# Optimization experiments

Measured on AMD Instinct MI355X. Metric: run time of the kernel, lower is better.

## Reference

```python
import jax, jax.numpy as jnp
import numpy as np

B, D, H = 8192, 512, 512


def _linear_init(key, out_dim, in_dim, bias=True):
    # torch nn.Linear default: U(-1/sqrt(in_dim), 1/sqrt(in_dim)) for W and b
    k1, k2 = jax.random.split(key)
    bound = 1.0 / np.sqrt(in_dim)
    W = jax.random.uniform(k1, (out_dim, in_dim), jnp.float32, -bound, bound)
    if not bias:
        return W
    b = jax.random.uniform(k2, (out_dim,), jnp.float32, -bound, bound)
    return W, b


def setup_inputs() -> dict:
    key = jax.random.key(0)
    ks = jax.random.split(key, 16)
    x = jax.random.normal(ks[0], (B, D), jnp.float32)
    delta_t = jax.random.uniform(ks[1], (B, 1), jnp.float32)
    hidden = jax.random.normal(ks[2], (B, H), jnp.float32)
    cell_s = jax.random.normal(ks[3], (B, H), jnp.float32)
    Wii, bii = _linear_init(ks[4], H, D)
    Whi, bhi = _linear_init(ks[5], H, H)
    Wig, big = _linear_init(ks[6], H, D)
    Whg, bhg = _linear_init(ks[7], H, H)
    Wio, bio = _linear_init(ks[8], H, D)
    Who, bho = _linear_init(ks[9], H, H)
    Wto, bto = _linear_init(ks[10], H, 1)
    Wco, bco = _linear_init(ks[11], H, H)
    Wit1, bit1 = _linear_init(ks[12], H, D)
    Wtt1 = _linear_init(ks[13], H, 1, bias=False)
    Wit2, bit2 = _linear_init(ks[14], H, D)
    Wtt2 = _linear_init(ks[15], H, 1, bias=False)
    return dict(x=x, delta_t=delta_t, hidden=hidden, cell_s=cell_s,
                Wii=Wii, bii=bii, Whi=Whi, bhi=bhi, Wig=Wig, big=big,
                Whg=Whg, bhg=bhg, Wio=Wio, bio=bio, Who=Who, bho=bho,
                Wto=Wto, bto=bto, Wco=Wco, bco=bco, Wit1=Wit1, bit1=bit1,
                Wtt1=Wtt1, Wit2=Wit2, bit2=bit2, Wtt2=Wtt2)


def _lin(a, W, b=None):
    y = a @ W.T
    return y if b is None else y + b


def reference(x, delta_t, hidden, cell_s,
              Wii, bii, Whi, bhi, Wig, big, Whg, bhg,
              Wio, bio, Who, bho, Wto, bto, Wco, bco,
              Wit1, bit1, Wtt1, Wit2, bit2, Wtt2):
    sig, tanh = jax.nn.sigmoid, jnp.tanh
    tm1 = sig(_lin(x, Wit1, bit1) + sig(_lin(delta_t, Wtt1)))
    tm2 = sig(_lin(x, Wit2, bit2) + sig(_lin(delta_t, Wtt2)))
    im = sig(_lin(x, Wii, bii) + _lin(hidden, Whi, bhi))
    cur_in = tanh(_lin(x, Wig, big) + _lin(hidden, Whg, bhg))
    it1 = im * tm1
    cm_t = (1.0 - it1) * cell_s + it1 * cur_in
    cm = (1.0 - im) * cell_s + im * tm2 * cur_in
    om = sig(_lin(x, Wio, bio) + _lin(delta_t, Wto, bto)
             + _lin(hidden, Who, bho) + _lin(cm_t, Wco, bco))
    hm = om * tanh(cm_t)
    return (hm, cm)
```

## Files before the change

kernel.cpp:

```cpp
#include <hip/hip_runtime.h>
#include <hip/hip_bf16.h>
#include <stdint.h>

#define B_SZ 8192
#define D_SZ 512
#define H_SZ 512
#define KC 1024
#define NPRE 2560

typedef __attribute__((ext_vector_type(8))) __bf16 bf16x8;
typedef __attribute__((ext_vector_type(4))) float f32x4;

__device__ __forceinline__ unsigned short f2bf(float f) {
  unsigned u = __builtin_bit_cast(unsigned, f);
  u += 0x7FFFu + ((u >> 16) & 1u);
  return (unsigned short)(u >> 16);
}
__device__ __forceinline__ float bf2f(unsigned short h) {
  unsigned u = ((unsigned)h) << 16;
  return __builtin_bit_cast(float, u);
}
__device__ __forceinline__ float sigf(float x) { return 1.0f / (1.0f + __expf(-x)); }

__device__ __forceinline__ void async_ld16(const unsigned short* g, unsigned short* l) {
  __builtin_amdgcn_global_load_lds(
      (const __attribute__((address_space(1))) unsigned int*)g,
      (__attribute__((address_space(3))) unsigned int*)l, 16, 0, 0);
}

struct WSrcs { const float* wx[5]; const float* wh[3]; const float* wco; };

__global__ void pack_all(const float* __restrict__ x, const float* __restrict__ h, WSrcs ws,
                         unsigned short* __restrict__ Ab, unsigned short* __restrict__ Wall,
                         unsigned short* __restrict__ Wcob) {
  int i = (blockIdx.x * 256 + threadIdx.x) * 4;
  const int XH = B_SZ * KC;
  const float* s;
  unsigned short* d;
  if (i < XH) {
    int b = i >> 10, c = i & 1023;
    s = (c < 512) ? (x + (size_t)b * 512 + c) : (h + (size_t)b * 512 + (c - 512));
    d = Ab + i;
  } else if (i < XH + NPRE * KC) {
    int j = i - XH;
    int row = j >> 10, c = j & 1023;
    int gate = row >> 9, r = row & 511;
    d = Wall + j;
    if (c < 512) {
      s = ws.wx[gate] + (size_t)r * 512 + c;
    } else if (gate >= 2) {
      s = ws.wh[gate - 2] + (size_t)r * 512 + (c - 512);
    } else {
      return;
    }
  } else {
    int j = i - XH - NPRE * KC;
    s = ws.wco + j;
    d = Wcob + j;
  }
  float4 v = *(const float4*)s;
  ushort4 o; o.x = f2bf(v.x); o.y = f2bf(v.y); o.z = f2bf(v.z); o.w = f2bf(v.w);
  *(ushort4*)d = o;
}

__global__ __launch_bounds__(256, 2) void gemm_t12(
    const unsigned short* __restrict__ A, const unsigned short* __restrict__ W,
    unsigned short* __restrict__ T12,
    const float* __restrict__ bit1, const float* __restrict__ Wtt1,
    const float* __restrict__ bit2, const float* __restrict__ Wtt2,
    const float* __restrict__ delta_t) {
  __shared__ bf16x8 sA[128 * 8];
  __shared__ bf16x8 sW[128 * 8];
  const int tid  = threadIdx.x;
  const int wave = tid >> 6, lane = tid & 63;
  const int ln15 = lane & 15, kq = lane >> 4;
  const int wr = wave >> 1, wc = wave & 1;
  const long bm = (long)blockIdx.y * 128;
  const long bn = (long)blockIdx.x * 128;

  f32x4 acc[4][4];
#pragma unroll
  for (int i = 0; i < 4; ++i)
#pragma unroll
    for (int j = 0; j < 4; ++j) acc[i][j] = (f32x4){0.f, 0.f, 0.f, 0.f};

  const int swb = ln15 & 7;
  for (int kt = 0; kt < 8; ++kt) {
    const int k0 = kt << 6;
    __syncthreads();
#pragma unroll
    for (int it = 0; it < 4; ++it) {
      int f   = it * 256 + tid;
      int row = f >> 3;
      int col = ((f & 7) ^ (row & 7)) << 3;
      int ldsc = it * 256 + wave * 64;
      async_ld16(A + (size_t)(bm + row) * KC + k0 + col, (unsigned short*)sA + (size_t)ldsc * 8);
      async_ld16(W + (size_t)(bn + row) * KC + k0 + col, (unsigned short*)sW + (size_t)ldsc * 8);
    }
    __syncthreads();
#pragma unroll
    for (int ko = 0; ko < 2; ++ko) {
      const int q = (ko * 4 + kq) ^ swb;
      bf16x8 af[4], wf[4];
#pragma unroll
      for (int t = 0; t < 4; ++t)
        af[t] = sA[(wr * 64 + t * 16 + ln15) * 8 + q];
#pragma unroll
      for (int t = 0; t < 4; ++t)
        wf[t] = sW[(wc * 64 + t * 16 + ln15) * 8 + q];
#pragma unroll
      for (int i = 0; i < 4; ++i)
#pragma unroll
        for (int j = 0; j < 4; ++j)
          acc[i][j] = __builtin_amdgcn_mfma_f32_16x16x32_bf16(af[i], wf[j], acc[i][j], 0, 0, 0);
    }
  }
  const float* bitp = (bn < 512) ? bit1 : bit2;
  const float* wttp = (bn < 512) ? Wtt1 : Wtt2;
#pragma unroll
  for (int i = 0; i < 4; ++i) {
    const long r0 = bm + wr * 64 + i * 16 + kq * 4;
#pragma unroll
    for (int j = 0; j < 4; ++j) {
      const long c = bn + wc * 64 + j * 16 + ln15;
      const int hc = (int)c & 511;
      const float bv = bitp[hc], wv = wttp[hc];
#pragma unroll
      for (int r = 0; r < 4; ++r) {
        const long row = r0 + r;
        float v = sigf(acc[i][j][r] + bv + sigf(delta_t[row] * wv));
        T12[(size_t)row * 1024 + c] = f2bf(v);
      }
    }
  }
}

__global__ __launch_bounds__(384, 2) void igo_gate(
    const unsigned short* __restrict__ A, const unsigned short* __restrict__ Wigo,
    const unsigned short* __restrict__ T12,
    const float* __restrict__ delta_t, const float* __restrict__ cell_s,
    const float* __restrict__ bii, const float* __restrict__ bhi,
    const float* __restrict__ big, const float* __restrict__ bhg,
    const float* __restrict__ bio, const float* __restrict__ bho,
    const float* __restrict__ Wto, const float* __restrict__ bto,
    const float* __restrict__ bco,
    float* __restrict__ out_cm, unsigned short* __restrict__ cmt_b,
    unsigned short* __restrict__ ao_b) {
  __shared__ __align__(16) unsigned short sBuf[24576];
  const int tid  = threadIdx.x;
  const int wave = tid >> 6, lane = tid & 63;
  const int ln15 = lane & 15, kq = lane >> 4;
  const int mh   = wave / 3, slot = wave % 3;
  const long bm  = (long)blockIdx.y * 128;
  const int  bn64 = blockIdx.x * 64;

  f32x4 acc[4][4];
#pragma unroll
  for (int i = 0; i < 4; ++i)
#pragma unroll
    for (int j = 0; j < 4; ++j) acc[i][j] = (f32x4){0.f, 0.f, 0.f, 0.f};

  const int swb = ln15 & 7;
  bf16x8* chunks = (bf16x8*)sBuf;

  for (int kt = 0; kt < 16; ++kt) {
    const int k0 = kt << 6;
    __syncthreads();
#pragma unroll
    for (int it = 0; it < 7; ++it) {
      int idx = it * 384 + tid;
      if (idx < 2560) {
        int t   = idx >> 9;
        int f   = idx & 511;
        int row = f >> 3;
        int col = ((f & 7) ^ (row & 7)) << 3;
        const unsigned short* src;
        if (t < 2) src = A    + (size_t)(bm + t * 64 + row) * KC + k0 + col;
        else       src = Wigo + (size_t)((t - 2) * 512 + bn64 + row) * KC + k0 + col;
        async_ld16(src, sBuf + (size_t)idx * 8);
      }
    }
    __syncthreads();
#pragma unroll
    for (int ko = 0; ko < 2; ++ko) {
      const int q = (ko * 4 + kq) ^ swb;
      bf16x8 af[4], wf[4];
#pragma unroll
      for (int t = 0; t < 4; ++t)
        af[t] = chunks[mh * 512 + (t * 16 + ln15) * 8 + q];
#pragma unroll
      for (int t = 0; t < 4; ++t)
        wf[t] = chunks[(2 + slot) * 512 + (t * 16 + ln15) * 8 + q];
#pragma unroll
      for (int i = 0; i < 4; ++i)
#pragma unroll
        for (int j = 0; j < 4; ++j)
          acc[i][j] = __builtin_amdgcn_mfma_f32_16x16x32_bf16(af[i], wf[j], acc[i][j], 0, 0, 0);
    }
  }

  __syncthreads();
#pragma unroll
  for (int i = 0; i < 4; ++i)
#pragma unroll
    for (int j = 0; j < 4; ++j)
#pragma unroll
      for (int r = 0; r < 4; ++r) {
        int row = i * 16 + kq * 4 + r;
        int col = j * 16 + ln15;
        sBuf[(size_t)(mh * 3 + slot) * 4096 + row * 64 + col] = f2bf(acc[i][j][r]);
      }
  __syncthreads();

  for (int e4 = tid * 4; e4 < 8192; e4 += 384 * 4) {
    int emh = e4 >> 12;
    int rc  = e4 & 4095;
    int row = rc >> 6;
    int col = rc & 63;
    long b  = bm + emh * 64 + row;
    int  h  = bn64 + col;
    ushort4 uai = *(const ushort4*)(sBuf + (size_t)(emh * 3 + 0) * 4096 + row * 64 + col);
    ushort4 uag = *(const ushort4*)(sBuf + (size_t)(emh * 3 + 1) * 4096 + row * 64 + col);
    ushort4 uao = *(const ushort4*)(sBuf + (size_t)(emh * 3 + 2) * 4096 + row * 64 + col);
    ushort4 ut1 = *(const ushort4*)(T12 + (size_t)b * 1024 + h);
    ushort4 ut2 = *(const ushort4*)(T12 + (size_t)b * 1024 + 512 + h);
    float4 cs   = *(const float4*)(cell_s + (size_t)b * 512 + h);
    float4 vbii = *(const float4*)(bii + h), vbhi = *(const float4*)(bhi + h);
    float4 vbig = *(const float4*)(big + h), vbhg = *(const float4*)(bhg + h);
    float4 vbio = *(const float4*)(bio + h), vbho = *(const float4*)(bho + h);
    float4 vWto = *(const float4*)(Wto + h), vbto = *(const float4*)(bto + h);
    float4 vbco = *(const float4*)(bco + h);
    float dtb   = delta_t[b];

    float4 ocm; ushort4 ocmt, oao;
#pragma unroll
    for (int l = 0; l < 4; ++l) {
      float ai = bf2f(((const unsigned short*)&uai)[l]) + ((const float*)&vbii)[l] + ((const float*)&vbhi)[l];
      float ag = bf2f(((const unsigned short*)&uag)[l]) + ((const float*)&vbig)[l] + ((const float*)&vbhg)[l];
      float ao = bf2f(((const unsigned short*)&uao)[l]) + ((const float*)&vbio)[l] + ((const float*)&vbho)[l]
               + dtb * ((const float*)&vWto)[l] + ((const float*)&vbto)[l] + ((const float*)&vbco)[l];
      float t1 = bf2f(((const unsigned short*)&ut1)[l]);
      float t2 = bf2f(((const unsigned short*)&ut2)[l]);
      float im = sigf(ai);
      float g  = tanhf(ag);
      float csl = ((const float*)&cs)[l];
      float it1 = im * t1;
      float cmt = (1.f - it1) * csl + it1 * g;
      float cm  = (1.f - im) * csl + im * t2 * g;
      ((float*)&ocm)[l] = cm;
      ((unsigned short*)&ocmt)[l] = f2bf(cmt);
      ((unsigned short*)&oao)[l]  = f2bf(ao);
    }
    *(float4*)(out_cm + (size_t)b * 512 + h) = ocm;
    *(ushort4*)(cmt_b + (size_t)b * 512 + h) = ocmt;
    *(ushort4*)(ao_b  + (size_t)b * 512 + h) = oao;
  }
}

__global__ __launch_bounds__(256, 2) void gemm_out(
    const unsigned short* __restrict__ A , const unsigned short* __restrict__ W ,
    const unsigned short* __restrict__ AO, float* __restrict__ out_hm) {
  __shared__ bf16x8 sA[128 * 8];
  __shared__ bf16x8 sW[128 * 8];
  const int tid  = threadIdx.x;
  const int wave = tid >> 6, lane = tid & 63;
  const int ln15 = lane & 15, kq = lane >> 4;
  const int wr = wave >> 1, wc = wave & 1;
  const long bm = (long)blockIdx.y * 128;
  const long bn = (long)blockIdx.x * 128;
  const int swb = ln15 & 7;

  f32x4 acc[4][4];
#pragma unroll
  for (int i = 0; i < 4; ++i)
#pragma unroll
    for (int j = 0; j < 4; ++j) acc[i][j] = (f32x4){0.f, 0.f, 0.f, 0.f};

  for (int kt = 0; kt < 8; ++kt) {
    const int k0 = kt << 6;
    __syncthreads();
#pragma unroll
    for (int it = 0; it < 4; ++it) {
      int f   = it * 256 + tid;
      int row = f >> 3;
      int col = ((f & 7) ^ (row & 7)) << 3;
      int ldsc = it * 256 + wave * 64;
      async_ld16(A + (size_t)(bm + row) * H_SZ + k0 + col, (unsigned short*)sA + (size_t)ldsc * 8);
      async_ld16(W + (size_t)(bn + row) * H_SZ + k0 + col, (unsigned short*)sW + (size_t)ldsc * 8);
    }
    __syncthreads();
#pragma unroll
    for (int ko = 0; ko < 2; ++ko) {
      const int q = (ko * 4 + kq) ^ swb;
      bf16x8 af[4], wf[4];
#pragma unroll
      for (int t = 0; t < 4; ++t)
        af[t] = sA[(wr * 64 + t * 16 + ln15) * 8 + q];
#pragma unroll
      for (int t = 0; t < 4; ++t)
        wf[t] = sW[(wc * 64 + t * 16 + ln15) * 8 + q];
#pragma unroll
      for (int i = 0; i < 4; ++i)
#pragma unroll
        for (int j = 0; j < 4; ++j)
          acc[i][j] = __builtin_amdgcn_mfma_f32_16x16x32_bf16(af[i], wf[j], acc[i][j], 0, 0, 0);
    }
  }
#pragma unroll
  for (int i = 0; i < 4; ++i) {
    const long r0 = bm + wr * 64 + i * 16 + kq * 4;
#pragma unroll
    for (int j = 0; j < 4; ++j) {
      const long c = bn + wc * 64 + j * 16 + ln15;
#pragma unroll
      for (int r = 0; r < 4; ++r) {
        long row = r0 + r;
        size_t idx = (size_t)row * H_SZ + c;
        float ao  = bf2f(AO[idx]);
        float om  = sigf(ao + acc[i][j][r]);
        float cmt = bf2f(A[idx]);
        out_hm[idx] = om * tanhf(cmt);
      }
    }
  }
}

extern "C" void kernel_launch(void* const* d_in, const int* in_sizes, int n_in,
                              void* d_out, int out_size, void* d_ws, size_t ws_size,
                              hipStream_t stream) {
  const float* x    = (const float*)d_in[0];
  const float* dt   = (const float*)d_in[1];
  const float* hid  = (const float*)d_in[2];
  const float* cell = (const float*)d_in[3];
  const float* Wii  = (const float*)d_in[4];
  const float* bii  = (const float*)d_in[5];
  const float* Whi  = (const float*)d_in[6];
  const float* bhi  = (const float*)d_in[7];
  const float* Wig  = (const float*)d_in[8];
  const float* big  = (const float*)d_in[9];
  const float* Whg  = (const float*)d_in[10];
  const float* bhg  = (const float*)d_in[11];
  const float* Wio  = (const float*)d_in[12];
  const float* bio  = (const float*)d_in[13];
  const float* Who  = (const float*)d_in[14];
  const float* bho  = (const float*)d_in[15];
  const float* Wto  = (const float*)d_in[16];
  const float* bto  = (const float*)d_in[17];
  const float* Wco  = (const float*)d_in[18];
  const float* bco  = (const float*)d_in[19];
  const float* Wit1 = (const float*)d_in[20];
  const float* bit1 = (const float*)d_in[21];
  const float* Wtt1 = (const float*)d_in[22];
  const float* Wit2 = (const float*)d_in[23];
  const float* bit2 = (const float*)d_in[24];
  const float* Wtt2 = (const float*)d_in[25];

  char* wp = (char*)d_ws;
  unsigned short* Ab   = (unsigned short*)wp; wp += (size_t)B_SZ * KC * 2;
  unsigned short* Wall = (unsigned short*)wp; wp += (size_t)NPRE * KC * 2;
  unsigned short* Wcob = (unsigned short*)wp; wp += (size_t)H_SZ * H_SZ * 2;
  unsigned short* T12  = (unsigned short*)wp; wp += (size_t)B_SZ * 1024 * 2;
  unsigned short* Cmtb = (unsigned short*)wp; wp += (size_t)B_SZ * H_SZ * 2;
  unsigned short* AOb  = (unsigned short*)wp; wp += (size_t)B_SZ * H_SZ * 2;

  float* out = (float*)d_out;

  WSrcs wsrc;
  wsrc.wx[0] = Wit1; wsrc.wx[1] = Wit2; wsrc.wx[2] = Wii; wsrc.wx[3] = Wig; wsrc.wx[4] = Wio;
  wsrc.wh[0] = Whi;  wsrc.wh[1] = Whg;  wsrc.wh[2] = Who; wsrc.wco = Wco;
  const int pack_elems = B_SZ * KC + NPRE * KC + H_SZ * H_SZ;
  pack_all<<<pack_elems / 4 / 256, 256, 0, stream>>>(x, hid, wsrc, Ab, Wall, Wcob);

  gemm_t12<<<dim3(8, 64), 256, 0, stream>>>(Ab, Wall, T12, bit1, Wtt1, bit2, Wtt2, dt);

  const unsigned short* Wigo = Wall + (size_t)1024 * KC;
  igo_gate<<<dim3(8, 64), 384, 0, stream>>>(
      Ab, Wigo, T12, dt, cell, bii, bhi, big, bhg, bio, bho, Wto, bto, bco,
      out + (size_t)B_SZ * H_SZ, Cmtb, AOb);

  gemm_out<<<dim3(4, 64), 256, 0, stream>>>(Cmtb, Wcob, AOb, out);
}
```

Before: 226.6 us.

## Fuse time-gate GEMM into gate kernel and use fast rcp-based activations

Removes the separate gemm_t12 kernel and computes the two time-gate projections inside igo_gate. It grows the block to 10 waves, with 5 weight slots per row half, and slots 0-1 only accumulate over the x half of K. This drops the T12 intermediate write and read and one launch, and applies the time-gate sigmoids in the fused epilogue. Sigmoid and tanh now use hardware reciprocal approximations instead of division and tanhf, which trades some accuracy for fewer instructions. The epilogue is split into two passes over row halves to fit LDS, and the two time-gate waves sit idle during the h half of K, which costs load balance and occupancy.

Result: slower. 251.6 us (+11.0%).

```diff
diff --git a/kernel.cpp b/kernel.cpp
--- a/kernel.cpp
+++ b/kernel.cpp
@@ -20,7 +20,13 @@
   unsigned u = ((unsigned)h) << 16;
   return __builtin_bit_cast(float, u);
 }
-__device__ __forceinline__ float sigf(float x) { return 1.0f / (1.0f + __expf(-x)); }
+__device__ __forceinline__ float sigf(float x) {
+  return __builtin_amdgcn_rcpf(1.0f + __expf(-x));
+}
+__device__ __forceinline__ float tanh_fast(float x) {
+  float e = __expf(-2.0f * x);
+  return (1.0f - e) * __builtin_amdgcn_rcpf(1.0f + e);
+}
 
 __device__ __forceinline__ void async_ld16(const unsigned short* g, unsigned short* l) {
   __builtin_amdgcn_global_load_lds(
@@ -63,94 +69,23 @@
   *(ushort4*)d = o;
 }
 
-__global__ __launch_bounds__(256, 2) void gemm_t12(
-    const unsigned short* __restrict__ A, const unsigned short* __restrict__ W,
-    unsigned short* __restrict__ T12,
-    const float* __restrict__ bit1, const float* __restrict__ Wtt1,
-    const float* __restrict__ bit2, const float* __restrict__ Wtt2,
-    const float* __restrict__ delta_t) {
-  __shared__ bf16x8 sA[128 * 8];
-  __shared__ bf16x8 sW[128 * 8];
-  const int tid  = threadIdx.x;
-  const int wave = tid >> 6, lane = tid & 63;
-  const int ln15 = lane & 15, kq = lane >> 4;
-  const int wr = wave >> 1, wc = wave & 1;
-  const long bm = (long)blockIdx.y * 128;
-  const long bn = (long)blockIdx.x * 128;
-
-  f32x4 acc[4][4];
-#pragma unroll
-  for (int i = 0; i < 4; ++i)
-#pragma unroll
-    for (int j = 0; j < 4; ++j) acc[i][j] = (f32x4){0.f, 0.f, 0.f, 0.f};
-
-  const int swb = ln15 & 7;
-  for (int kt = 0; kt < 8; ++kt) {
-    const int k0 = kt << 6;
-    __syncthreads();
-#pragma unroll
-    for (int it = 0; it < 4; ++it) {
-      int f   = it * 256 + tid;
-      int row = f >> 3;
-      int col = ((f & 7) ^ (row & 7)) << 3;
-      int ldsc = it * 256 + wave * 64;
-      async_ld16(A + (size_t)(bm + row) * KC + k0 + col, (unsigned short*)sA + (size_t)ldsc * 8);
-      async_ld16(W + (size_t)(bn + row) * KC + k0 + col, (unsigned short*)sW + (size_t)ldsc * 8);
-    }
-    __syncthreads();
-#pragma unroll
-    for (int ko = 0; ko < 2; ++ko) {
-      const int q = (ko * 4 + kq) ^ swb;
-      bf16x8 af[4], wf[4];
-#pragma unroll
-      for (int t = 0; t < 4; ++t)
-        af[t] = sA[(wr * 64 + t * 16 + ln15) * 8 + q];
-#pragma unroll
-      for (int t = 0; t < 4; ++t)
-        wf[t] = sW[(wc * 64 + t * 16 + ln15) * 8 + q];
-#pragma unroll
-      for (int i = 0; i < 4; ++i)
-#pragma unroll
-        for (int j = 0; j < 4; ++j)
-          acc[i][j] = __builtin_amdgcn_mfma_f32_16x16x32_bf16(af[i], wf[j], acc[i][j], 0, 0, 0);
-    }
-  }
-  const float* bitp = (bn < 512) ? bit1 : bit2;
-  const float* wttp = (bn < 512) ? Wtt1 : Wtt2;
-#pragma unroll
-  for (int i = 0; i < 4; ++i) {
-    const long r0 = bm + wr * 64 + i * 16 + kq * 4;
-#pragma unroll
-    for (int j = 0; j < 4; ++j) {
-      const long c = bn + wc * 64 + j * 16 + ln15;
-      const int hc = (int)c & 511;
-      const float bv = bitp[hc], wv = wttp[hc];
-#pragma unroll
-      for (int r = 0; r < 4; ++r) {
-        const long row = r0 + r;
-        float v = sigf(acc[i][j][r] + bv + sigf(delta_t[row] * wv));
-        T12[(size_t)row * 1024 + c] = f2bf(v);
-      }
-    }
-  }
-}
-
-__global__ __launch_bounds__(384, 2) void igo_gate(
-    const unsigned short* __restrict__ A, const unsigned short* __restrict__ Wigo,
-    const unsigned short* __restrict__ T12,
+__global__ __launch_bounds__(640, 2) void igo_gate(
+    const unsigned short* __restrict__ A, const unsigned short* __restrict__ Wall,
     const float* __restrict__ delta_t, const float* __restrict__ cell_s,
     const float* __restrict__ bii, const float* __restrict__ bhi,
     const float* __restrict__ big, const float* __restrict__ bhg,
     const float* __restrict__ bio, const float* __restrict__ bho,
     const float* __restrict__ Wto, const float* __restrict__ bto,
     const float* __restrict__ bco,
+    const float* __restrict__ bit1, const float* __restrict__ Wtt1,
+    const float* __restrict__ bit2, const float* __restrict__ Wtt2,
     float* __restrict__ out_cm, unsigned short* __restrict__ cmt_b,
     unsigned short* __restrict__ ao_b) {
-  __shared__ __align__(16) unsigned short sBuf[24576];
+  __shared__ __align__(16) unsigned short sBuf[28672];
   const int tid  = threadIdx.x;
   const int wave = tid >> 6, lane = tid & 63;
   const int ln15 = lane & 15, kq = lane >> 4;
-  const int mh   = wave / 3, slot = wave % 3;
+  const int mh   = wave / 5, slot = wave % 5;
   const long bm  = (long)blockIdx.y * 128;
   const int  bn64 = blockIdx.x * 64;
 
@@ -166,94 +101,100 @@
   for (int kt = 0; kt < 16; ++kt) {
     const int k0 = kt << 6;
     __syncthreads();
-#pragma unroll
-    for (int it = 0; it < 7; ++it) {
-      int idx = it * 384 + tid;
-      if (idx < 2560) {
-        int t   = idx >> 9;
-        int f   = idx & 511;
-        int row = f >> 3;
-        int col = ((f & 7) ^ (row & 7)) << 3;
-        const unsigned short* src;
-        if (t < 2) src = A    + (size_t)(bm + t * 64 + row) * KC + k0 + col;
-        else       src = Wigo + (size_t)((t - 2) * 512 + bn64 + row) * KC + k0 + col;
-        async_ld16(src, sBuf + (size_t)idx * 8);
+    const int cnt = (kt < 8) ? 3584 : 2560;
+    for (int idx = tid; idx < cnt; idx += 640) {
+      int t_lin = idx >> 9;
+      int f     = idx & 511;
+      int tile  = (kt < 8) ? t_lin : (t_lin < 2 ? t_lin : t_lin + 2);
+      int row = f >> 3;
+      int col = ((f & 7) ^ (row & 7)) << 3;
+      const unsigned short* src;
+      if (tile < 2) src = A    + (size_t)(bm + tile * 64 + row) * KC + k0 + col;
+      else          src = Wall + (size_t)((tile - 2) * 512 + bn64 + row) * KC + k0 + col;
+      async_ld16(src, sBuf + (size_t)(tile * 512 + f) * 8);
+    }
+    __syncthreads();
+    if (kt < 8 || slot >= 2) {
+#pragma unroll
+      for (int ko = 0; ko < 2; ++ko) {
+        const int q = (ko * 4 + kq) ^ swb;
+        bf16x8 af[4], wf[4];
+#pragma unroll
+        for (int t = 0; t < 4; ++t)
+          af[t] = chunks[mh * 512 + (t * 16 + ln15) * 8 + q];
+#pragma unroll
+        for (int t = 0; t < 4; ++t)
+          wf[t] = chunks[(2 + slot) * 512 + (t * 16 + ln15) * 8 + q];
+#pragma unroll
+        for (int i = 0; i < 4; ++i)
+#pragma unroll
+          for (int j = 0; j < 4; ++j)
+            acc[i][j] = __builtin_amdgcn_mfma_f32_16x16x32_bf16(af[i], wf[j], acc[i][j], 0, 0, 0);
       }
     }
-    __syncthreads();
-#pragma unroll
-    for (int ko = 0; ko < 2; ++ko) {
-      const int q = (ko * 4 + kq) ^ swb;
-      bf16x8 af[4], wf[4];
-#pragma unroll
-      for (int t = 0; t < 4; ++t)
-        af[t] = chunks[mh * 512 + (t * 16 + ln15) * 8 + q];
-#pragma unroll
-      for (int t = 0; t < 4; ++t)
-        wf[t] = chunks[(2 + slot) * 512 + (t * 16 + ln15) * 8 + q];
+  }
+
+  for (int mh_e = 0; mh_e < 2; ++mh_e) {
+    __syncthreads();
+    if (mh == mh_e) {
 #pragma unroll
       for (int i = 0; i < 4; ++i)
 #pragma unroll
         for (int j = 0; j < 4; ++j)
-          acc[i][j] = __builtin_amdgcn_mfma_f32_16x16x32_bf16(af[i], wf[j], acc[i][j], 0, 0, 0);
-    }
-  }
-
-  __syncthreads();
-#pragma unroll
-  for (int i = 0; i < 4; ++i)
-#pragma unroll
-    for (int j = 0; j < 4; ++j)
-#pragma unroll
-      for (int r = 0; r < 4; ++r) {
-        int row = i * 16 + kq * 4 + r;
-        int col = j * 16 + ln15;
-        sBuf[(size_t)(mh * 3 + slot) * 4096 + row * 64 + col] = f2bf(acc[i][j][r]);
+#pragma unroll
+          for (int r = 0; r < 4; ++r) {
+            int row = i * 16 + kq * 4 + r;
+            int col = j * 16 + ln15;
+            sBuf[(size_t)slot * 4096 + row * 64 + col] = f2bf(acc[i][j][r]);
+          }
+    }
+    __syncthreads();
+    for (int v = tid; v < 1024; v += 640) {
+      int row = v >> 4;
+      int c4  = (v & 15) << 2;
+      long b  = bm + mh_e * 64 + row;
+      int  h  = bn64 + c4;
+      int  lo = row * 64 + c4;
+      ushort4 ut1 = *(const ushort4*)(sBuf + 0 * 4096 + lo);
+      ushort4 ut2 = *(const ushort4*)(sBuf + 1 * 4096 + lo);
+      ushort4 uai = *(const ushort4*)(sBuf + 2 * 4096 + lo);
+      ushort4 uag = *(const ushort4*)(sBuf + 3 * 4096 + lo);
+      ushort4 uao = *(const ushort4*)(sBuf + 4 * 4096 + lo);
+      float4 cs   = *(const float4*)(cell_s + (size_t)b * 512 + h);
+      float4 vbii = *(const float4*)(bii + h), vbhi = *(const float4*)(bhi + h);
+      float4 vbig = *(const float4*)(big + h), vbhg = *(const float4*)(bhg + h);
+      float4 vbio = *(const float4*)(bio + h), vbho = *(const float4*)(bho + h);
+      float4 vWto = *(const float4*)(Wto + h), vbto = *(const float4*)(bto + h);
+      float4 vbco = *(const float4*)(bco + h);
+      float4 vbt1 = *(const float4*)(bit1 + h), vwt1 = *(const float4*)(Wtt1 + h);
+      float4 vbt2 = *(const float4*)(bit2 + h), vwt2 = *(const float4*)(Wtt2 + h);
+      float dtb   = delta_t[b];
+
+      float4 ocm; ushort4 ocmt, oao;
+#pragma unroll
+      for (int l = 0; l < 4; ++l) {
+        float t1 = sigf(bf2f(((const unsigned short*)&ut1)[l]) + ((const float*)&vbt1)[l]
+                        + sigf(dtb * ((const float*)&vwt1)[l]));
+        float t2 = sigf(bf2f(((const unsigned short*)&ut2)[l]) + ((const float*)&vbt2)[l]
+                        + sigf(dtb * ((const float*)&vwt2)[l]));
+        float ai = bf2f(((const unsigned short*)&uai)[l]) + ((const float*)&vbii)[l] + ((const float*)&vbhi)[l];
+        float ag = bf2f(((const unsigned short*)&uag)[l]) + ((const float*)&vbig)[l] + ((const float*)&vbhg)[l];
+        float ao = bf2f(((const unsigned short*)&uao)[l]) + ((const float*)&vbio)[l] + ((const float*)&vbho)[l]
+                 + dtb * ((const float*)&vWto)[l] + ((const float*)&vbto)[l] + ((const float*)&vbco)[l];
+        float im = sigf(ai);
+        float g  = tanh_fast(ag);
+        float csl = ((const float*)&cs)[l];
+        float it1 = im * t1;
+        float cmt = (1.f - it1) * csl + it1 * g;
+        float cm  = (1.f - im) * csl + im * t2 * g;
+        ((float*)&ocm)[l] = cm;
+        ((unsigned short*)&ocmt)[l] = f2bf(cmt);
+        ((unsigned short*)&oao)[l]  = f2bf(ao);
       }
-  __syncthreads();
-
-  for (int e4 = tid * 4; e4 < 8192; e4 += 384 * 4) {
-    int emh = e4 >> 12;
-    int rc  = e4 & 4095;
-    int row = rc >> 6;
-    int col = rc & 63;
-    long b  = bm + emh * 64 + row;
-    int  h  = bn64 + col;
-    ushort4 uai = *(const ushort4*)(sBuf + (size_t)(emh * 3 + 0) * 4096 + row * 64 + col);
-    ushort4 uag = *(const ushort4*)(sBuf + (size_t)(emh * 3 + 1) * 4096 + row * 64 + col);
-    ushort4 uao = *(const ushort4*)(sBuf + (size_t)(emh * 3 + 2) * 4096 + row * 64 + col);
-    ushort4 ut1 = *(const ushort4*)(T12 + (size_t)b * 1024 + h);
-    ushort4 ut2 = *(const ushort4*)(T12 + (size_t)b * 1024 + 512 + h);
-    float4 cs   = *(const float4*)(cell_s + (size_t)b * 512 + h);
-    float4 vbii = *(const float4*)(bii + h), vbhi = *(const float4*)(bhi + h);
-    float4 vbig = *(const float4*)(big + h), vbhg = *(const float4*)(bhg + h);
-    float4 vbio = *(const float4*)(bio + h), vbho = *(const float4*)(bho + h);
-    float4 vWto = *(const float4*)(Wto + h), vbto = *(const float4*)(bto + h);
-    float4 vbco = *(const float4*)(bco + h);
-    float dtb   = delta_t[b];
-
-    float4 ocm; ushort4 ocmt, oao;
-#pragma unroll
-    for (int l = 0; l < 4; ++l) {
-      float ai = bf2f(((const unsigned short*)&uai)[l]) + ((const float*)&vbii)[l] + ((const float*)&vbhi)[l];
-      float ag = bf2f(((const unsigned short*)&uag)[l]) + ((const float*)&vbig)[l] + ((const float*)&vbhg)[l];
-      float ao = bf2f(((const unsigned short*)&uao)[l]) + ((const float*)&vbio)[l] + ((const float*)&vbho)[l]
-               + dtb * ((const float*)&vWto)[l] + ((const float*)&vbto)[l] + ((const float*)&vbco)[l];
-      float t1 = bf2f(((const unsigned short*)&ut1)[l]);
-      float t2 = bf2f(((const unsigned short*)&ut2)[l]);
-      float im = sigf(ai);
-      float g  = tanhf(ag);
-      float csl = ((const float*)&cs)[l];
-      float it1 = im * t1;
-      float cmt = (1.f - it1) * csl + it1 * g;
-      float cm  = (1.f - im) * csl + im * t2 * g;
-      ((float*)&ocm)[l] = cm;
-      ((unsigned short*)&ocmt)[l] = f2bf(cmt);
-      ((unsigned short*)&oao)[l]  = f2bf(ao);
-    }
-    *(float4*)(out_cm + (size_t)b * 512 + h) = ocm;
-    *(ushort4*)(cmt_b + (size_t)b * 512 + h) = ocmt;
-    *(ushort4*)(ao_b  + (size_t)b * 512 + h) = oao;
+      *(float4*)(out_cm + (size_t)b * 512 + h) = ocm;
+      *(ushort4*)(cmt_b + (size_t)b * 512 + h) = ocmt;
+      *(ushort4*)(ao_b  + (size_t)b * 512 + h) = oao;
+    }
   }
 }
 
@@ -319,7 +260,7 @@
         float ao  = bf2f(AO[idx]);
         float om  = sigf(ao + acc[i][j][r]);
         float cmt = bf2f(A[idx]);
-        out_hm[idx] = om * tanhf(cmt);
+        out_hm[idx] = om * tanh_fast(cmt);
       }
     }
   }
@@ -359,7 +300,6 @@
   unsigned short* Ab   = (unsigned short*)wp; wp += (size_t)B_SZ * KC * 2;
   unsigned short* Wall = (unsigned short*)wp; wp += (size_t)NPRE * KC * 2;
   unsigned short* Wcob = (unsigned short*)wp; wp += (size_t)H_SZ * H_SZ * 2;
-  unsigned short* T12  = (unsigned short*)wp; wp += (size_t)B_SZ * 1024 * 2;
   unsigned short* Cmtb = (unsigned short*)wp; wp += (size_t)B_SZ * H_SZ * 2;
   unsigned short* AOb  = (unsigned short*)wp; wp += (size_t)B_SZ * H_SZ * 2;
 
@@ -371,11 +311,9 @@
   const int pack_elems = B_SZ * KC + NPRE * KC + H_SZ * H_SZ;
   pack_all<<<pack_elems / 4 / 256, 256, 0, stream>>>(x, hid, wsrc, Ab, Wall, Wcob);
 
-  gemm_t12<<<dim3(8, 64), 256, 0, stream>>>(Ab, Wall, T12, bit1, Wtt1, bit2, Wtt2, dt);
-
-  const unsigned short* Wigo = Wall + (size_t)1024 * KC;
-  igo_gate<<<dim3(8, 64), 384, 0, stream>>>(
-      Ab, Wigo, T12, dt, cell, bii, bhi, big, bhg, bio, bho, Wto, bto, bco,
+  igo_gate<<<dim3(8, 64), 640, 0, stream>>>(
+      Ab, Wall, dt, cell, bii, bhi, big, bhg, bio, bho, Wto, bto, bco,
+      bit1, Wtt1, bit2, Wtt2,
       out + (size_t)B_SZ * H_SZ, Cmtb, AOb);
 
   gemm_out<<<dim3(4, 64), 256, 0, stream>>>(Cmtb, Wcob, AOb, out);
```
